# Performance work log

Measured on AMD Instinct MI355X. Metric: run time of the kernel, lower is better.

## Reference

```python
import jax, jax.numpy as jnp
import numpy as np

N_NODES = 500_000
N_EDGES = 4_000_000
N_GRAPHS = 5_000
C = 16          # hidden states
M = 32          # discrete node-label alphabet
N_GEN = 16      # number of mixture generators


def setup_inputs() -> dict:
    key = jax.random.key(0)
    k1, k2, k3, k4, k5 = jax.random.split(key, 5)
    x = jax.random.randint(k1, (N_NODES,), 0, M)
    edge_index = jax.random.randint(k2, (2, N_EDGES), 0, N_NODES)
    batch = jnp.sort(jax.random.randint(k3, (N_NODES,), 0, N_GRAPHS))
    # params initialized ~ U(-5, 5) as in nn.init.uniform_(..., a=-5, b=5)
    B = jax.random.uniform(k4, (C, M, N_GEN), minval=-5.0, maxval=5.0)
    Pi = jax.random.uniform(k5, (C, N_GEN), minval=-5.0, maxval=5.0)
    return {"x": x, "edge_index": edge_index, "batch": batch, "B": B, "Pi": Pi}


def reference(x, edge_index, batch, B, Pi):
    # CGMM forward with the as-constructed single CGMMLayer_0.
    # edge_index is a forward arg of CGMM but unused by layer 0.
    sm_B = jax.nn.softmax(B, axis=1)        # softmax over M per (C, gen)
    sm_Pi = jax.nn.softmax(Pi, axis=0)      # softmax over C per gen
    # sm_B[:, x] -> (C, N, n_gen); permute(1, 0, 2) -> (N, C, n_gen)
    emissions = jnp.transpose(sm_B[:, x], (1, 0, 2))
    numerator = sm_Pi[None, :, :] * emissions            # (N, C, n_gen)
    posterior = numerator / numerator.sum(axis=1, keepdims=True)
    lik_node = (posterior * jnp.log(numerator)).sum(axis=1)  # (N, n_gen)
    lik_graph = jax.ops.segment_sum(lik_node, batch, num_segments=N_GRAPHS)
    # CGMM stacks per-layer likelihoods on dim=1 and negates -> (G, 1, n_gen)
    return -lik_graph[:, None, :]
```

## Files before the change

### kernel.cpp

```cpp
#include <hip/hip_runtime.h>
#include <hip/hip_bf16.h>

#define CC 16
#define MM 32
#define NGEN 16
#define TLP 17

__global__ void __launch_bounds__(256) cgmm_prep_kernel(
        const float* __restrict__ B,
        const float* __restrict__ Pi,
        const int* __restrict__ batch,
        float* __restrict__ T,
        int* __restrict__ offs,
        int n_nodes, int n_graphs) {
    if (blockIdx.x == 0) {
        __shared__ float E[CC][MM][NGEN];
        __shared__ float Acg[CC][NGEN];
        __shared__ float Lcg[CC][NGEN];
        __shared__ float ePi[CC][NGEN];
        __shared__ float dPi[NGEN];

        const int tid = threadIdx.x;
        const int c = tid >> 4, g = tid & 15;

        float s = 0.f;
        #pragma unroll
        for (int m = 0; m < MM; ++m) {
            const float e = expf(B[(c * MM + m) * NGEN + g]);
            E[c][m][g] = e;
            s += e;
        }
        const float dB = s;
        ePi[c][g] = expf(Pi[c * NGEN + g]);
        __syncthreads();
        if (tid < NGEN) {
            float t = 0.f;
            #pragma unroll
            for (int cc = 0; cc < CC; ++cc) t += ePi[cc][tid];
            dPi[tid] = t;
        }
        __syncthreads();
        Acg[c][g] = ePi[c][g] / (dPi[g] * dB);
        Lcg[c][g] = Pi[c * NGEN + g] - logf(dPi[g]) - logf(dB);
        __syncthreads();

        #pragma unroll
        for (int r = 0; r < 2; ++r) {
            const int m = (tid >> 4) + r * 16;
            float ssum = 0.f, lsum = 0.f;
            #pragma unroll
            for (int cc = 0; cc < CC; ++cc) {
                const float ne = Acg[cc][g] * E[cc][m][g];
                ssum += ne;
                lsum += ne * (Lcg[cc][g] + B[(cc * MM + m) * NGEN + g]);
            }
            T[m * NGEN + g] = lsum / ssum;
        }
    } else {
        const int idx = (blockIdx.x - 1) * blockDim.x + threadIdx.x;
        const int stride = (gridDim.x - 1) * blockDim.x;
        for (int n = idx; n < n_nodes; n += stride) {
            const int b = batch[n];
            const int prev = (n == 0) ? -1 : batch[n - 1];
            for (int gph = prev + 1; gph <= b; ++gph) offs[gph] = n;
            if (n == n_nodes - 1)
                for (int gph = b + 1; gph <= n_graphs; ++gph) offs[gph] = n_nodes;
        }
    }
}

__global__ void __launch_bounds__(256) cgmm_graph_kernel(
        const int* __restrict__ x,
        const int* __restrict__ offs,
        const float* __restrict__ T,
        float* __restrict__ out,
        int n_graphs) {
    __shared__ float Tl[MM * TLP];
    const int tid = threadIdx.x;
    for (int i = tid; i < MM * NGEN; i += 256)
        Tl[(i >> 4) * TLP + (i & 15)] = T[i];

    const int lane = tid & 63;
    const int gid = blockIdx.x * 4 + (tid >> 6);
    __syncthreads();

    if (gid < n_graphs) {
        const int start = offs[gid];
        const int end   = offs[gid + 1];
        const int g = lane & 15;
        const int chunk = lane >> 4;

        float acc = 0.f;
        int n = start + chunk;
        for (; n + 12 < end; n += 16) {
            const int x0 = x[n], x1 = x[n + 4], x2 = x[n + 8], x3 = x[n + 12];
            acc += Tl[x0 * TLP + g];
            acc += Tl[x1 * TLP + g];
            acc += Tl[x2 * TLP + g];
            acc += Tl[x3 * TLP + g];
        }
        for (; n < end; n += 4) acc += Tl[x[n] * TLP + g];

        acc += __shfl_down(acc, 32);
        acc += __shfl_down(acc, 16);

        if (lane < NGEN) out[gid * NGEN + lane] = -acc;
    }
}

extern "C" void kernel_launch(void* const* d_in, const int* in_sizes, int n_in,
                              void* d_out, int out_size, void* d_ws, size_t ws_size,
                              hipStream_t stream) {
    const int* x     = (const int*)d_in[0];
    const int* batch = (const int*)d_in[2];
    const float* B   = (const float*)d_in[3];
    const float* Pi  = (const float*)d_in[4];
    float* out       = (float*)d_out;
    float* T         = (float*)d_ws;
    int*   offs      = (int*)((char*)d_ws + 4096);

    const int n_nodes  = in_sizes[0];
    const int n_graphs = out_size / NGEN;

    hipLaunchKernelGGL(cgmm_prep_kernel, dim3(256), dim3(256), 0, stream,
                       B, Pi, batch, T, offs, n_nodes, n_graphs);
    hipLaunchKernelGGL(cgmm_graph_kernel, dim3((n_graphs + 3) / 4), dim3(256), 0, stream,
                       x, offs, T, out, n_graphs);
}
```

Before: 13.96 us.

## Fuse prep and graph kernels, replace offset scan with per-wave ballot binary search

Merges the two launches into one kernel. Every block recomputes the 32x16 likelihood table from B and Pi in shared memory. Each wave finds its graph's node range by a 32-way ballot search over the sorted batch array, which replaces the full pass over batch that wrote an offsets array. This removes a launch, the global scan and the workspace round trip. In exchange, every block redundantly loads 32KB of B and evaluates several thousand expf, and the search issues serial dependent global loads.

```diff
diff --git a/kernel.cpp b/kernel.cpp
--- a/kernel.cpp
+++ b/kernel.cpp
@@ -5,88 +5,105 @@
 #define MM 32
 #define NGEN 16
 #define TLP 17
+#define GPB 8
 
-__global__ void __launch_bounds__(256) cgmm_prep_kernel(
+__global__ void __launch_bounds__(512) cgmm_fused_kernel(
+        const int* __restrict__ x,
+        const int* __restrict__ batch,
         const float* __restrict__ B,
         const float* __restrict__ Pi,
-        const int* __restrict__ batch,
-        float* __restrict__ T,
-        int* __restrict__ offs,
+        float* __restrict__ out,
         int n_nodes, int n_graphs) {
-    if (blockIdx.x == 0) {
-        __shared__ float E[CC][MM][NGEN];
-        __shared__ float Acg[CC][NGEN];
-        __shared__ float Lcg[CC][NGEN];
-        __shared__ float ePi[CC][NGEN];
-        __shared__ float dPi[NGEN];
+    __shared__ float Bs[CC * MM * NGEN];
+    __shared__ float ePiS[CC][NGEN];
+    __shared__ float dPiS[NGEN];
+    __shared__ float Acg[CC][NGEN];
+    __shared__ float Lcg[CC][NGEN];
+    __shared__ float Tl[MM * TLP];
 
-        const int tid = threadIdx.x;
-        const int c = tid >> 4, g = tid & 15;
+    const int tid  = threadIdx.x;
+    const int wave = tid >> 6;
+    const int lane = tid & 63;
+    const int gid  = blockIdx.x * GPB + wave;
 
+    int start = 0, end = 0;
+    if (gid < n_graphs) {
+        const int half = lane >> 5;
+        const int li   = lane & 31;
+        const int target = gid + half;
+
+        int lo = 0, hi = n_nodes;
+        while (hi - lo > 32) {
+            const int step = (hi - lo) >> 5;
+            const int p = lo + li * step;
+            const bool c = batch[p] < target;
+            const unsigned mask = (unsigned)(__ballot(c) >> (half << 5));
+            const int k = __popc(mask);
+            if (k == 0) {
+                hi = lo;
+            } else {
+                const int nhi = (k < 32) ? (lo + k * step) : hi;
+                lo = lo + (k - 1) * step + 1;
+                hi = nhi;
+            }
+        }
+        int bound;
+        {
+            const int p = lo + li;
+            const bool c = (p < hi) && (batch[p] < target);
+            const unsigned mask = (unsigned)(__ballot(c) >> (half << 5));
+            bound = lo + __popc(mask);
+        }
+        start = __shfl(bound, 0);
+        end   = __shfl(bound, 32);
+    }
+
+    {
+        const float4* B4  = (const float4*)B;
+        float4*       Bs4 = (float4*)Bs;
+        #pragma unroll
+        for (int i = 0; i < 4; ++i)
+            Bs4[tid + i * 512] = B4[tid + i * 512];
+        if (tid < CC * NGEN)
+            ePiS[tid >> 4][tid & 15] = expf(Pi[tid]);
+    }
+    __syncthreads();
+
+    float dB = 0.f;
+    const int c0 = tid >> 4, g0 = tid & 15;
+    if (tid < CC * NGEN) {
+        #pragma unroll
+        for (int m = 0; m < MM; ++m)
+            dB += expf(Bs[(c0 * MM + m) * NGEN + g0]);
+    } else if (tid < CC * NGEN + NGEN) {
+        const int gg = tid - CC * NGEN;
         float s = 0.f;
         #pragma unroll
-        for (int m = 0; m < MM; ++m) {
-            const float e = expf(B[(c * MM + m) * NGEN + g]);
-            E[c][m][g] = e;
-            s += e;
+        for (int cc = 0; cc < CC; ++cc) s += ePiS[cc][gg];
+        dPiS[gg] = s;
+    }
+    __syncthreads();
+    if (tid < CC * NGEN) {
+        Acg[c0][g0] = ePiS[c0][g0] / (dPiS[g0] * dB);
+        Lcg[c0][g0] = Pi[tid] - logf(dPiS[g0]) - logf(dB);
+    }
+    __syncthreads();
+    {
+        const int m = tid >> 4;
+        const int g = tid & 15;
+        float ssum = 0.f, lsum = 0.f;
+        #pragma unroll
+        for (int cc = 0; cc < CC; ++cc) {
+            const float b  = Bs[(cc * MM + m) * NGEN + g];
+            const float ne = Acg[cc][g] * expf(b);
+            ssum += ne;
+            lsum += ne * (Lcg[cc][g] + b);
         }
-        const float dB = s;
-        ePi[c][g] = expf(Pi[c * NGEN + g]);
-        __syncthreads();
-        if (tid < NGEN) {
-            float t = 0.f;
-            #pragma unroll
-            for (int cc = 0; cc < CC; ++cc) t += ePi[cc][tid];
-            dPi[tid] = t;
-        }
-        __syncthreads();
-        Acg[c][g] = ePi[c][g] / (dPi[g] * dB);
-        Lcg[c][g] = Pi[c * NGEN + g] - logf(dPi[g]) - logf(dB);
-        __syncthreads();
-
-        #pragma unroll
-        for (int r = 0; r < 2; ++r) {
-            const int m = (tid >> 4) + r * 16;
-            float ssum = 0.f, lsum = 0.f;
-            #pragma unroll
-            for (int cc = 0; cc < CC; ++cc) {
-                const float ne = Acg[cc][g] * E[cc][m][g];
-                ssum += ne;
-                lsum += ne * (Lcg[cc][g] + B[(cc * MM + m) * NGEN + g]);
-            }
-            T[m * NGEN + g] = lsum / ssum;
-        }
-    } else {
-        const int idx = (blockIdx.x - 1) * blockDim.x + threadIdx.x;
-        const int stride = (gridDim.x - 1) * blockDim.x;
-        for (int n = idx; n < n_nodes; n += stride) {
-            const int b = batch[n];
-            const int prev = (n == 0) ? -1 : batch[n - 1];
-            for (int gph = prev + 1; gph <= b; ++gph) offs[gph] = n;
-            if (n == n_nodes - 1)
-                for (int gph = b + 1; gph <= n_graphs; ++gph) offs[gph] = n_nodes;
-        }
+        Tl[m * TLP + g] = lsum / ssum;
     }
-}
-
-__global__ void __launch_bounds__(256) cgmm_graph_kernel(
-        const int* __restrict__ x,
-        const int* __restrict__ offs,
-        const float* __restrict__ T,
-        float* __restrict__ out,
-        int n_graphs) {
-    __shared__ float Tl[MM * TLP];
-    const int tid = threadIdx.x;
-    for (int i = tid; i < MM * NGEN; i += 256)
-        Tl[(i >> 4) * TLP + (i & 15)] = T[i];
-
-    const int lane = tid & 63;
-    const int gid = blockIdx.x * 4 + (tid >> 6);
     __syncthreads();
 
     if (gid < n_graphs) {
-        const int start = offs[gid];
-        const int end   = offs[gid + 1];
         const int g = lane & 15;
         const int chunk = lane >> 4;
 
@@ -116,14 +133,11 @@
     const float* B   = (const float*)d_in[3];
     const float* Pi  = (const float*)d_in[4];
     float* out       = (float*)d_out;
-    float* T         = (float*)d_ws;
-    int*   offs      = (int*)((char*)d_ws + 4096);
 
     const int n_nodes  = in_sizes[0];
     const int n_graphs = out_size / NGEN;
 
-    hipLaunchKernelGGL(cgmm_prep_kernel, dim3(256), dim3(256), 0, stream,
-                       B, Pi, batch, T, offs, n_nodes, n_graphs);
-    hipLaunchKernelGGL(cgmm_graph_kernel, dim3((n_graphs + 3) / 4), dim3(256), 0, stream,
-                       x, offs, T, out, n_graphs);
+    hipLaunchKernelGGL(cgmm_fused_kernel,
+                       dim3((n_graphs + GPB - 1) / GPB), dim3(512), 0, stream,
+                       x, batch, B, Pi, out, n_nodes, n_graphs);
 }
```

Measured after the change: 15.50 us. 1.11x slower.

## Build per-graph label histograms with LDS atomics, then contract with table

Applied to the files above, without the earlier changes.

The graph kernel now counts label occurrences per graph in a shared-memory histogram, filled by coalesced 64-wide loads of x and LDS atomic adds. Each graph's output is then computed as a 32x16 histogram-times-table product instead of one table lookup per node per generator. Blocks grow to 512 threads covering eight graphs, and the table load overlaps the histogram build. This removes the per-node, per-generator LDS gathers and the 4-way strided x reads, at the cost of atomic contention on the 32 bins and summing integer counts multiplied by the table rather than accumulating individual floats.

```diff
diff --git a/kernel.cpp b/kernel.cpp
--- a/kernel.cpp
+++ b/kernel.cpp
@@ -5,6 +5,7 @@
 #define MM 32
 #define NGEN 16
 #define TLP 17
+#define GPB 8
 
 __global__ void __launch_bounds__(256) cgmm_prep_kernel(
         const float* __restrict__ B,
@@ -69,41 +70,46 @@
     }
 }
 
-__global__ void __launch_bounds__(256) cgmm_graph_kernel(
+__global__ void __launch_bounds__(512) cgmm_graph_kernel(
         const int* __restrict__ x,
         const int* __restrict__ offs,
         const float* __restrict__ T,
         float* __restrict__ out,
         int n_graphs) {
     __shared__ float Tl[MM * TLP];
-    const int tid = threadIdx.x;
-    for (int i = tid; i < MM * NGEN; i += 256)
-        Tl[(i >> 4) * TLP + (i & 15)] = T[i];
+    __shared__ int hist[GPB][MM];
 
+    const int tid  = threadIdx.x;
+    const int wave = tid >> 6;
     const int lane = tid & 63;
-    const int gid = blockIdx.x * 4 + (tid >> 6);
+    const int gid  = blockIdx.x * GPB + wave;
+
+    if (tid < MM * NGEN)
+        Tl[(tid >> 4) * TLP + (tid & 15)] = T[tid];
+    if (lane < MM)
+        hist[wave][lane] = 0;
+
+    int start = 0, end = 0;
+    if (gid < n_graphs) {
+        start = offs[gid];
+        end   = offs[gid + 1];
+    }
+    for (int n = start + lane; n < end; n += 64)
+        atomicAdd(&hist[wave][x[n]], 1);
+
     __syncthreads();
 
     if (gid < n_graphs) {
-        const int start = offs[gid];
-        const int end   = offs[gid + 1];
         const int g = lane & 15;
-        const int chunk = lane >> 4;
-
+        const int q = lane >> 4;
         float acc = 0.f;
-        int n = start + chunk;
-        for (; n + 12 < end; n += 16) {
-            const int x0 = x[n], x1 = x[n + 4], x2 = x[n + 8], x3 = x[n + 12];
-            acc += Tl[x0 * TLP + g];
-            acc += Tl[x1 * TLP + g];
-            acc += Tl[x2 * TLP + g];
-            acc += Tl[x3 * TLP + g];
+        #pragma unroll
+        for (int j = 0; j < 8; ++j) {
+            const int m = q * 8 + j;
+            acc += (float)hist[wave][m] * Tl[m * TLP + g];
         }
-        for (; n < end; n += 4) acc += Tl[x[n] * TLP + g];
-
         acc += __shfl_down(acc, 32);
         acc += __shfl_down(acc, 16);
-
         if (lane < NGEN) out[gid * NGEN + lane] = -acc;
     }
 }
@@ -124,6 +130,7 @@
 
     hipLaunchKernelGGL(cgmm_prep_kernel, dim3(256), dim3(256), 0, stream,
                        B, Pi, batch, T, offs, n_nodes, n_graphs);
-    hipLaunchKernelGGL(cgmm_graph_kernel, dim3((n_graphs + 3) / 4), dim3(256), 0, stream,
+    hipLaunchKernelGGL(cgmm_graph_kernel,
+                       dim3((n_graphs + GPB - 1) / GPB), dim3(512), 0, stream,
                        x, offs, T, out, n_graphs);
 }
```

Result: faster. 12.55 us (median of 2 runs) (-10.1%).
